# Performance work log

Hardware: AMD Instinct MI355X
Metric: run time of the kernel (lower is better)

The kernel has to match this reference:

```python
import jax, jax.numpy as jnp
import numpy as np

N_NODES = 100000
N_EDGES = 1600000
D = 128  # 2 * config.out_channels with config.out_channels = 64


def setup_inputs() -> dict:
    key = jax.random.key(0)
    k1, k2, k3, k4 = jax.random.split(key, 4)
    x_in = jax.random.normal(k1, (N_NODES, D), dtype=jnp.float32)
    x_out = jax.random.normal(k2, (N_NODES, D), dtype=jnp.float32)
    edge_index = jax.random.randint(k3, (2, N_EDGES), 0, N_NODES, dtype=jnp.int64)
    # nn.Bilinear(D, D, 1, bias=False) weight: [out_features=1, D, D]
    W = jax.random.normal(k4, (1, D, D), dtype=jnp.float32) * (1.0 / np.sqrt(D))
    return {"x_in": x_in, "x_out": x_out, "edge_index": edge_index, "W": W}


def reference(x_in, x_out, edge_index, W):
    # Gather edge endpoint features (irregular access)
    a = x_out[edge_index[0]]          # [E, D]
    b = x_in[edge_index[1]]           # [E, D]
    # Bilinear form with single output: value_e = a_e^T W0 b_e
    W0 = W[0]                         # [D, D]
    aW = a @ W0                       # [E, D]
    value = jnp.sum(aW * b, axis=-1)  # [E]
    return jax.nn.sigmoid(value)
```

## Files before the change

### kernel.cpp

```cpp
#include <hip/hip_runtime.h>
#include <hip/hip_fp16.h>
#include <math.h>

#define D 128

typedef _Float16 f16x8 __attribute__((ext_vector_type(8)));
typedef float    f32x4 __attribute__((ext_vector_type(4)));
typedef _Float16 h2_t  __attribute__((ext_vector_type(2)));

__device__ __forceinline__ float dot2acc(unsigned ua, unsigned ub, float c) {
#if __has_builtin(__builtin_amdgcn_fdot2)
  return __builtin_amdgcn_fdot2(__builtin_bit_cast(h2_t, ua),
                                __builtin_bit_cast(h2_t, ub), c, false);
#else
  __half2 a = __builtin_bit_cast(__half2, ua);
  __half2 b = __builtin_bit_cast(__half2, ub);
  float2 fa = __half22float2(a), fb = __half22float2(b);
  return fmaf(fa.x, fb.x, fmaf(fa.y, fb.y, c));
#endif
}

__device__ __forceinline__ unsigned pack2(float x, float y) {
  __half2 h;
  h.x = __float2half_rn(x);
  h.y = __float2half_rn(y);
  return __builtin_bit_cast(unsigned, h);
}

__global__ __launch_bounds__(256) void convert_f16_kernel(
    const float* __restrict__ x, __half* __restrict__ xh, int n4)
{
  int i = blockIdx.x * 256 + threadIdx.x;
  if (i >= n4) return;
  float4 v = ((const float4*)x)[i];
  uint2 u;
  u.x = pack2(v.x, v.y);
  u.y = pack2(v.z, v.w);
  ((uint2*)xh)[i] = u;
}

__global__ __launch_bounds__(256) void transpose_w_kernel(
    const float* __restrict__ W, __half* __restrict__ Wt)
{
  int o = blockIdx.x * 256 + threadIdx.x;
  if (o >= D * D) return;
  int k = o >> 7;
  int n = o & 127;
  Wt[n * D + k] = __float2half_rn(W[o]);
}

__global__ __launch_bounds__(256) void gemm_mfma_kernel(
    const float* __restrict__ X, const __half* __restrict__ Wt,
    __half* __restrict__ Y, int N)
{
  __shared__ __align__(16) __half sA[128 * 128];
  __shared__ __align__(16) __half sB[128 * 128];

  const int tid  = threadIdx.x;
  const int row0 = blockIdx.x * 128;

  #pragma unroll
  for (int i = 0; i < 16; i++) {
    int idx = tid + i * 256;
    int q   = idx & 31;
    int r   = idx >> 5;
    int gr  = row0 + r;
    float4 v = make_float4(0.f, 0.f, 0.f, 0.f);
    if (gr < N) v = *(const float4*)(X + (size_t)gr * D + q * 4);
    uint2 u;
    u.x = pack2(v.x, v.y);
    u.y = pack2(v.z, v.w);
    int g   = q >> 1;
    int sub = q & 1;
    int off = r * 128 + (((g + r) & 15) << 3) + (sub << 2);
    *(uint2*)(sA + off) = u;
  }
  #pragma unroll
  for (int i = 0; i < 8; i++) {
    int idx = tid + i * 256;
    int g   = idx & 15;
    int n   = idx >> 4;
    uint4 v = *(const uint4*)(Wt + n * 128 + g * 8);
    int off = n * 128 + (((g + n) & 15) << 3);
    *(uint4*)(sB + off) = v;
  }
  __syncthreads();

  const int wave = tid >> 6;
  const int lane = tid & 63;
  const int m    = lane & 15;
  const int quad = lane >> 4;

  f32x4 acc[2][8];
  #pragma unroll
  for (int rt = 0; rt < 2; rt++)
    #pragma unroll
    for (int ct = 0; ct < 8; ct++)
      acc[rt][ct] = (f32x4){0.f, 0.f, 0.f, 0.f};

  #pragma unroll
  for (int ks = 0; ks < 4; ks++) {
    const int g = ks * 4 + quad;
    f16x8 bfrag[8];
    #pragma unroll
    for (int ct = 0; ct < 8; ct++) {
      int n = ct * 16 + m;
      bfrag[ct] = *(const f16x8*)(sB + n * 128 + (((g + n) & 15) << 3));
    }
    #pragma unroll
    for (int rt = 0; rt < 2; rt++) {
      int r = wave * 32 + rt * 16 + m;
      f16x8 afrag = *(const f16x8*)(sA + r * 128 + (((g + r) & 15) << 3));
      #pragma unroll
      for (int ct = 0; ct < 8; ct++)
        acc[rt][ct] = __builtin_amdgcn_mfma_f32_16x16x32_f16(
            afrag, bfrag[ct], acc[rt][ct], 0, 0, 0);
    }
  }

  #pragma unroll
  for (int rt = 0; rt < 2; rt++) {
    #pragma unroll
    for (int reg = 0; reg < 4; reg++) {
      int gr = row0 + wave * 32 + rt * 16 + quad * 4 + reg;
      if (gr < N) {
        __half* yrow = Y + (size_t)gr * D;
        #pragma unroll
        for (int ct = 0; ct < 8; ct++)
          yrow[ct * 16 + m] = __float2half_rn(acc[rt][ct][reg]);
      }
    }
  }
}

__global__ __launch_bounds__(256) void edge_dot2_kernel(
    const __half* __restrict__ Yh, const __half* __restrict__ Xh,
    const int* __restrict__ idx, float* __restrict__ out, int E)
{
  long long gid = (long long)blockIdx.x * 256 + threadIdx.x;
  int slot = (int)(gid >> 4);
  int l    = (int)(gid & 15);
  int e0 = slot * 2;
  if (e0 >= E) return;
  int e1 = e0 + 1;
  bool has1 = (e1 < E);

  int s0 = idx[e0];
  int d0 = idx[E + e0];
  int s1 = has1 ? idx[e1] : s0;
  int d1 = has1 ? idx[E + e1] : d0;

  uint4 a0 = ((const uint4*)(Yh + (size_t)s0 * D))[l];
  uint4 b0 = ((const uint4*)(Xh + (size_t)d0 * D))[l];
  uint4 a1 = ((const uint4*)(Yh + (size_t)s1 * D))[l];
  uint4 b1 = ((const uint4*)(Xh + (size_t)d1 * D))[l];

  float p = 0.f, q = 0.f;
  p = dot2acc(a0.x, b0.x, p);  q = dot2acc(a1.x, b1.x, q);
  p = dot2acc(a0.y, b0.y, p);  q = dot2acc(a1.y, b1.y, q);
  p = dot2acc(a0.z, b0.z, p);  q = dot2acc(a1.z, b1.z, q);
  p = dot2acc(a0.w, b0.w, p);  q = dot2acc(a1.w, b1.w, q);

  p += __shfl_xor(p, 8);  q += __shfl_xor(q, 8);
  p += __shfl_xor(p, 4);  q += __shfl_xor(q, 4);
  p += __shfl_xor(p, 2);  q += __shfl_xor(q, 2);
  p += __shfl_xor(p, 1);  q += __shfl_xor(q, 1);

  if (l == 0) {
    float2 o;
    o.x = 1.0f / (1.0f + __expf(-p));
    o.y = 1.0f / (1.0f + __expf(-q));
    if (has1) *(float2*)(out + e0) = o;
    else      out[e0] = o.x;
  }
}

__global__ __launch_bounds__(256) void edge_bilinear_direct_kernel(
    const float* __restrict__ Xout, const float* __restrict__ Xin,
    const float* __restrict__ W, const int* __restrict__ idx,
    float* __restrict__ out, int E)
{
  long long gid = (long long)blockIdx.x * 256 + threadIdx.x;
  int e = (int)(gid >> 6);
  if (e >= E) return;
  int l = (int)(gid & 63);

  int src = idx[e];
  int dst = idx[E + e];
  const float* a = Xout + (size_t)src * D;
  const float* b = Xin  + (size_t)dst * D;

  float s = 0.f;
  #pragma unroll
  for (int kk = 0; kk < 2; kk++) {
    int k = l + kk * 64;
    float ak = a[k];
    float t = 0.f;
    #pragma unroll 8
    for (int j = 0; j < D; j++) t = fmaf(W[(size_t)k * D + j], b[j], t);
    s = fmaf(ak, t, s);
  }
  #pragma unroll
  for (int off = 32; off >= 1; off >>= 1) s += __shfl_xor(s, off);
  if (l == 0) out[e] = 1.0f / (1.0f + __expf(-s));
}

extern "C" void kernel_launch(void* const* d_in, const int* in_sizes, int n_in,
                              void* d_out, int out_size, void* d_ws, size_t ws_size,
                              hipStream_t stream) {
  const float* x_in  = (const float*)d_in[0];
  const float* x_out = (const float*)d_in[1];
  const int*   eidx  = (const int*)d_in[2];
  const float* W     = (const float*)d_in[3];
  float* out = (float*)d_out;

  const int N = in_sizes[0] / D;
  const int E = in_sizes[2] / 2;

  const size_t half_rows = (size_t)N * D * sizeof(__half);

  if (ws_size >= 2 * half_rows) {
    __half* Yh = (__half*)d_ws;
    __half* Xh = (__half*)((char*)d_ws + half_rows);
    __half* Wt;
    if (ws_size >= 2 * half_rows + (size_t)D * D * sizeof(__half))
      Wt = (__half*)((char*)d_ws + 2 * half_rows);
    else
      Wt = (__half*)d_out;

    int n4 = N * D / 4;
    convert_f16_kernel<<<(n4 + 255) / 256, 256, 0, stream>>>(x_in, Xh, n4);

    transpose_w_kernel<<<(D * D + 255) / 256, 256, 0, stream>>>(W, Wt);

    dim3 g1((N + 127) / 128);
    gemm_mfma_kernel<<<g1, 256, 0, stream>>>(x_out, Wt, Yh, N);

    long long slots = (E + 1) / 2;
    long long total = slots * 16;
    dim3 g2((unsigned)((total + 255) / 256));
    edge_dot2_kernel<<<g2, 256, 0, stream>>>(Yh, Xh, eidx, out, E);
  } else {
    long long total = (long long)E * 64;
    dim3 g((unsigned)((total + 255) / 256));
    edge_bilinear_direct_kernel<<<g, 256, 0, stream>>>(x_out, x_in, W, eidx, out, E);
  }
}
```

Before: 259.3 us.

## Fuse convert, W transpose and GEMM into one prep kernel with staged output

Merges the x_in fp16 conversion, the W transpose and the MFMA GEMM into a single launch. Extra blocks beyond the GEMM blocks run a grid-stride conversion loop, so conversion overlaps with the GEMM. Each GEMM block now loads and transposes W into shared memory itself. The GEMM output is staged through LDS so global stores are coalesced 16-byte writes instead of scattered 2-byte ones. This removes two launches and the Wt round trip, but every GEMM block redoes the strided W transpose with scalar LDS stores.

```diff
diff --git a/kernel.cpp b/kernel.cpp
--- a/kernel.cpp
+++ b/kernel.cpp
@@ -3,6 +3,7 @@
 #include <math.h>
 
 #define D 128
+#define CONV_BLOCKS 1024
 
 typedef _Float16 f16x8 __attribute__((ext_vector_type(8)));
 typedef float    f32x4 __attribute__((ext_vector_type(4)));
@@ -27,36 +28,37 @@
   return __builtin_bit_cast(unsigned, h);
 }
 
-__global__ __launch_bounds__(256) void convert_f16_kernel(
-    const float* __restrict__ x, __half* __restrict__ xh, int n4)
-{
-  int i = blockIdx.x * 256 + threadIdx.x;
-  if (i >= n4) return;
-  float4 v = ((const float4*)x)[i];
-  uint2 u;
-  u.x = pack2(v.x, v.y);
-  u.y = pack2(v.z, v.w);
-  ((uint2*)xh)[i] = u;
-}
-
-__global__ __launch_bounds__(256) void transpose_w_kernel(
-    const float* __restrict__ W, __half* __restrict__ Wt)
-{
-  int o = blockIdx.x * 256 + threadIdx.x;
-  if (o >= D * D) return;
-  int k = o >> 7;
-  int n = o & 127;
-  Wt[n * D + k] = __float2half_rn(W[o]);
-}
-
-__global__ __launch_bounds__(256) void gemm_mfma_kernel(
-    const float* __restrict__ X, const __half* __restrict__ Wt,
-    __half* __restrict__ Y, int N)
+__global__ __launch_bounds__(256) void prep_kernel(
+    const float* __restrict__ Xout, const float* __restrict__ Xin,
+    const float* __restrict__ W, __half* __restrict__ Yh,
+    __half* __restrict__ Xh, int N, int gemm_blocks)
 {
   __shared__ __align__(16) __half sA[128 * 128];
   __shared__ __align__(16) __half sB[128 * 128];
 
-  const int tid  = threadIdx.x;
+  const int tid = threadIdx.x;
+
+  if ((int)blockIdx.x >= gemm_blocks) {
+    const int cb = blockIdx.x - gemm_blocks;
+    const int n4 = N * (D / 4);
+    const int stride = CONV_BLOCKS * 256 * 4;
+    for (int base = (cb * 256 + tid) * 4; base < n4; base += stride) {
+      float4 v[4];
+      #pragma unroll
+      for (int j = 0; j < 4; j++)
+        if (base + j < n4) v[j] = ((const float4*)Xin)[base + j];
+      #pragma unroll
+      for (int j = 0; j < 4; j++)
+        if (base + j < n4) {
+          uint2 u;
+          u.x = pack2(v[j].x, v[j].y);
+          u.y = pack2(v[j].z, v[j].w);
+          ((uint2*)Xh)[base + j] = u;
+        }
+    }
+    return;
+  }
+
   const int row0 = blockIdx.x * 128;
 
   #pragma unroll
@@ -66,7 +68,7 @@
     int r   = idx >> 5;
     int gr  = row0 + r;
     float4 v = make_float4(0.f, 0.f, 0.f, 0.f);
-    if (gr < N) v = *(const float4*)(X + (size_t)gr * D + q * 4);
+    if (gr < N) v = *(const float4*)(Xout + (size_t)gr * D + q * 4);
     uint2 u;
     u.x = pack2(v.x, v.y);
     u.y = pack2(v.z, v.w);
@@ -76,13 +78,13 @@
     *(uint2*)(sA + off) = u;
   }
   #pragma unroll
-  for (int i = 0; i < 8; i++) {
-    int idx = tid + i * 256;
-    int g   = idx & 15;
-    int n   = idx >> 4;
-    uint4 v = *(const uint4*)(Wt + n * 128 + g * 8);
-    int off = n * 128 + (((g + n) & 15) << 3);
-    *(uint4*)(sB + off) = v;
+  for (int i = 0; i < 64; i++) {
+    int o = tid + i * 256;
+    int k = o >> 7;
+    int n = o & 127;
+    __half h = __float2half_rn(W[o]);
+    int gk = k >> 3;
+    sB[n * 128 + (((gk + n) & 15) << 3) + (k & 7)] = h;
   }
   __syncthreads();
 
@@ -118,18 +120,26 @@
     }
   }
 
-  #pragma unroll
-  for (int rt = 0; rt < 2; rt++) {
+  __syncthreads();
+  __half* sC = sA;
+  #pragma unroll
+  for (int rt = 0; rt < 2; rt++)
     #pragma unroll
     for (int reg = 0; reg < 4; reg++) {
-      int gr = row0 + wave * 32 + rt * 16 + quad * 4 + reg;
-      if (gr < N) {
-        __half* yrow = Y + (size_t)gr * D;
-        #pragma unroll
-        for (int ct = 0; ct < 8; ct++)
-          yrow[ct * 16 + m] = __float2half_rn(acc[rt][ct][reg]);
-      }
-    }
+      int r = wave * 32 + rt * 16 + quad * 4 + reg;
+      #pragma unroll
+      for (int ct = 0; ct < 8; ct++)
+        sC[r * 128 + ct * 16 + m] = __float2half_rn(acc[rt][ct][reg]);
+    }
+  __syncthreads();
+  #pragma unroll
+  for (int i = 0; i < 8; i++) {
+    int idx = tid + i * 256;
+    int r   = idx >> 4;
+    int gq  = idx & 15;
+    int gr  = row0 + r;
+    if (gr < N)
+      *(uint4*)(Yh + (size_t)gr * D + gq * 8) = *(const uint4*)(sC + r * 128 + gq * 8);
   }
 }
 
@@ -222,19 +232,10 @@
   if (ws_size >= 2 * half_rows) {
     __half* Yh = (__half*)d_ws;
     __half* Xh = (__half*)((char*)d_ws + half_rows);
-    __half* Wt;
-    if (ws_size >= 2 * half_rows + (size_t)D * D * sizeof(__half))
-      Wt = (__half*)((char*)d_ws + 2 * half_rows);
-    else
-      Wt = (__half*)d_out;
-
-    int n4 = N * D / 4;
-    convert_f16_kernel<<<(n4 + 255) / 256, 256, 0, stream>>>(x_in, Xh, n4);
-
-    transpose_w_kernel<<<(D * D + 255) / 256, 256, 0, stream>>>(W, Wt);
-
-    dim3 g1((N + 127) / 128);
-    gemm_mfma_kernel<<<g1, 256, 0, stream>>>(x_out, Wt, Yh, N);
+
+    int gemm_blocks = (N + 127) / 128;
+    dim3 g1(gemm_blocks + CONV_BLOCKS);
+    prep_kernel<<<g1, 256, 0, stream>>>(x_out, x_in, W, Yh, Xh, N, gemm_blocks);
 
     long long slots = (E + 1) / 2;
     long long total = slots * 16;
```

Result: faster. 252.9 us (-2.5%).
